# Kernel tuning notes

Hardware: AMD Instinct MI355X
Metric: run time of the kernel (lower is better)

Reference implementation:

```python
import jax, jax.numpy as jnp
import numpy as np

HEAD_DIM = 64
SCALE = HEAD_DIM ** -0.5
NUM_HEADS = 16


def setup_inputs() -> dict:
    key = jax.random.key(0)
    k1, k2, k3, k4 = jax.random.split(key, 4)
    dim = 1024
    query = jax.random.normal(k1, (8, 512, dim), dtype=jnp.float32)
    memory = jax.random.normal(k2, (8, 512, dim), dtype=jnp.float32)
    # nn.Linear weights are [out, in]; scale like default init
    W_Q = jax.random.normal(k3, (dim, dim), dtype=jnp.float32) * (dim ** -0.5)
    W_K = jax.random.normal(k4, (dim, dim), dtype=jnp.float32) * (dim ** -0.5)
    return {"query": query, "memory": memory, "W_Q": W_Q, "W_K": W_K}


def reference(query, memory, W_Q, W_K):
    # Q: [K, Lq, E], K: [B, Lk, E]  (E = H * D)
    Q = query @ W_Q.T
    Km = memory @ W_K.T
    Kb, Lq, E = Q.shape
    Bb, Lk, _ = Km.shape
    Qh = Q.reshape(Kb, Lq, NUM_HEADS, HEAD_DIM).transpose(0, 2, 1, 3)  # K H q D
    Kh = Km.reshape(Bb, Lk, NUM_HEADS, HEAD_DIM).transpose(0, 2, 1, 3)  # B H k D
    # logits: [B, K, H, q, k]
    logits = jnp.einsum('ahqd,bhkd->bahqk', Qh, Kh) * SCALE
    energies = jax.nn.logsumexp(logits, axis=-2) / SCALE  # [B, K, H, k]
    energies = energies.mean(axis=1)  # [B, H, k]
    return energies
```

## Files before the change

### kernel.cpp

```cpp
#include <hip/hip_runtime.h>
#include <hip/hip_bf16.h>

typedef short short8 __attribute__((ext_vector_type(8)));
typedef float f32x4 __attribute__((ext_vector_type(4)));
typedef unsigned short u16;

__device__ __forceinline__ unsigned short f2bf(float f) {
  unsigned int u = __float_as_uint(f);
  u += 0x7fffu + ((u >> 16) & 1u);
  return (unsigned short)(u >> 16);
}

__device__ __forceinline__ void glds16(const void* g, void* l) {
  __builtin_amdgcn_global_load_lds(
      (const __attribute__((address_space(1))) unsigned int*)g,
      (__attribute__((address_space(3))) unsigned int*)l, 16, 0, 0);
}

__global__ __launch_bounds__(256) void prep(const float4* __restrict__ q,
                                            const float4* __restrict__ m,
                                            const float4* __restrict__ wq,
                                            const float4* __restrict__ wk,
                                            ushort4* __restrict__ qb,
                                            ushort4* __restrict__ mb,
                                            ushort4* __restrict__ wqb,
                                            ushort4* __restrict__ wkb,
                                            float4* __restrict__ out0) {
  const int i = blockIdx.x * 256 + threadIdx.x;
  const float c = 0.18033688011112042f;
  if (i < 1048576) {
    float4 v = q[i];
    ushort4 o; o.x = f2bf(v.x); o.y = f2bf(v.y); o.z = f2bf(v.z); o.w = f2bf(v.w);
    qb[i] = o;
  } else if (i < 2097152) {
    float4 v = m[i - 1048576];
    ushort4 o; o.x = f2bf(v.x); o.y = f2bf(v.y); o.z = f2bf(v.z); o.w = f2bf(v.w);
    mb[i - 1048576] = o;
  } else if (i < 2359296) {
    float4 v = wq[i - 2097152];
    ushort4 o; o.x = f2bf(v.x * c); o.y = f2bf(v.y * c); o.z = f2bf(v.z * c); o.w = f2bf(v.w * c);
    wqb[i - 2097152] = o;
  } else if (i < 2621440) {
    float4 v = wk[i - 2359296];
    ushort4 o; o.x = f2bf(v.x); o.y = f2bf(v.y); o.z = f2bf(v.z); o.w = f2bf(v.w);
    wkb[i - 2359296] = o;
  } else if (i < 2637824) {
    out0[i - 2621440] = (float4){0.f, 0.f, 0.f, 0.f};
  }
}

__global__ __launch_bounds__(256) void gemm_bt2(const u16* __restrict__ A0,
                                                const u16* __restrict__ B0,
                                                u16* __restrict__ C0,
                                                const u16* __restrict__ A1,
                                                const u16* __restrict__ B1,
                                                u16* __restrict__ C1) {
  __shared__ u16 As[128 * 64];
  __shared__ u16 Bs[128 * 64];
  const u16* A = blockIdx.z ? A1 : A0;
  const u16* B = blockIdx.z ? B1 : B0;
  u16* C = blockIdx.z ? C1 : C0;
  const int t = threadIdx.x;
  const int lane = t & 63, wave = t >> 6;
  const int l15 = lane & 15, quad = lane >> 4;
  const int mb = blockIdx.y * 128, nb = blockIdx.x * 128;
  const int wm = (wave & 1) * 64, wn = (wave >> 1) * 64;

  const int srow = lane >> 3;
  const int scol = ((lane & 7) ^ srow) * 8;

  f32x4 acc[4][4];
#pragma unroll
  for (int i = 0; i < 4; i++)
#pragma unroll
    for (int j = 0; j < 4; j++) acc[i][j] = (f32x4){0.f, 0.f, 0.f, 0.f};

  for (int kb = 0; kb < 1024; kb += 64) {
#pragma unroll
    for (int j = 0; j < 4; j++) {
      const int mi_ = wave * 4 + j;
      const int row = mi_ * 8 + srow;
      glds16(A + (size_t)(mb + row) * 1024 + kb + scol, &As[mi_ * 512 + lane * 8]);
      glds16(B + (size_t)(nb + row) * 1024 + kb + scol, &Bs[mi_ * 512 + lane * 8]);
    }
    __syncthreads();
#pragma unroll
    for (int kk = 0; kk < 2; kk++) {
      const int cb = kk * 4;
      const int sw = l15 & 7;
      short8 af[4], bfr[4];
#pragma unroll
      for (int mi = 0; mi < 4; mi++)
        af[mi] = *(const short8*)&As[(wm + mi * 16 + l15) * 64 + ((cb + quad) ^ sw) * 8];
#pragma unroll
      for (int ni = 0; ni < 4; ni++)
        bfr[ni] = *(const short8*)&Bs[(wn + ni * 16 + l15) * 64 + ((cb + quad) ^ sw) * 8];
#pragma unroll
      for (int mi = 0; mi < 4; mi++)
#pragma unroll
        for (int ni = 0; ni < 4; ni++)
          acc[mi][ni] = __builtin_amdgcn_mfma_f32_16x16x32_bf16(
              af[mi], bfr[ni], acc[mi][ni], 0, 0, 0);
    }
    __syncthreads();
  }
#pragma unroll
  for (int mi = 0; mi < 4; mi++)
#pragma unroll
    for (int r = 0; r < 4; r++) {
      const int row = mb + wm + mi * 16 + quad * 4 + r;
      const size_t base = (size_t)row * 1024 + nb + wn;
#pragma unroll
      for (int ni = 0; ni < 4; ni++)
        C[base + ni * 16 + l15] = f2bf(acc[mi][ni][r]);
    }
}

__global__ __launch_bounds__(256) void attn_lse2(const u16* __restrict__ Qp,
                                                 const u16* __restrict__ Kp,
                                                 float* __restrict__ out) {
  __shared__ u16 qs[64 * 64];
  const int t = threadIdx.x;
  const int lane = t & 63, wave = t >> 6;
  const int l15 = lane & 15, quad = lane >> 4;
  const int kt = blockIdx.x & 1, aa = blockIdx.x >> 1;
  const int h = blockIdx.y, b = blockIdx.z;
  const int kwave = kt * 256 + wave * 64;

  short8 klo[4], khi[4];
#pragma unroll
  for (int tt = 0; tt < 4; tt++) {
    const short8* kg = (const short8*)(Kp + (size_t)(b * 512 + kwave + tt * 16 + l15) * 1024
                                       + h * 64 + quad * 8);
    klo[tt] = kg[0];
    khi[tt] = kg[4];
  }

  const int srow = lane >> 3;
  const int scol = ((lane & 7) ^ srow) * 8;
  const u16* qbase = Qp + (size_t)(aa * 512) * 1024 + h * 64;

  float cs0 = 0.f, cs1 = 0.f, cs2 = 0.f, cs3 = 0.f;

  for (int q0 = 0; q0 < 512; q0 += 64) {
    __syncthreads();
#pragma unroll
    for (int j = 0; j < 2; j++) {
      const int mi_ = wave * 2 + j;
      const int row = q0 + mi_ * 8 + srow;
      glds16(qbase + (size_t)row * 1024 + scol, &qs[mi_ * 512 + lane * 8]);
    }
    __syncthreads();
#pragma unroll
    for (int qt = 0; qt < 4; qt++) {
      const int rbase = (qt * 16 + l15) * 64;
      const int sw = l15 & 7;
      short8 alo = *(const short8*)&qs[rbase + (quad ^ sw) * 8];
      short8 ahi = *(const short8*)&qs[rbase + ((4 + quad) ^ sw) * 8];
      f32x4 ac0 = (f32x4){0.f, 0.f, 0.f, 0.f};
      f32x4 ac1 = ac0, ac2 = ac0, ac3 = ac0;
      ac0 = __builtin_amdgcn_mfma_f32_16x16x32_bf16(alo, klo[0], ac0, 0, 0, 0);
      ac0 = __builtin_amdgcn_mfma_f32_16x16x32_bf16(ahi, khi[0], ac0, 0, 0, 0);
      ac1 = __builtin_amdgcn_mfma_f32_16x16x32_bf16(alo, klo[1], ac1, 0, 0, 0);
      ac1 = __builtin_amdgcn_mfma_f32_16x16x32_bf16(ahi, khi[1], ac1, 0, 0, 0);
      ac2 = __builtin_amdgcn_mfma_f32_16x16x32_bf16(alo, klo[2], ac2, 0, 0, 0);
      ac2 = __builtin_amdgcn_mfma_f32_16x16x32_bf16(ahi, khi[2], ac2, 0, 0, 0);
      ac3 = __builtin_amdgcn_mfma_f32_16x16x32_bf16(alo, klo[3], ac3, 0, 0, 0);
      ac3 = __builtin_amdgcn_mfma_f32_16x16x32_bf16(ahi, khi[3], ac3, 0, 0, 0);
#pragma unroll
      for (int r = 0; r < 4; r++) {
        cs0 += exp2f(ac0[r]);
        cs1 += exp2f(ac1[r]);
        cs2 += exp2f(ac2[r]);
        cs3 += exp2f(ac3[r]);
      }
    }
  }
  cs0 += __shfl_xor(cs0, 16); cs0 += __shfl_xor(cs0, 32);
  cs1 += __shfl_xor(cs1, 16); cs1 += __shfl_xor(cs1, 32);
  cs2 += __shfl_xor(cs2, 16); cs2 += __shfl_xor(cs2, 32);
  cs3 += __shfl_xor(cs3, 16); cs3 += __shfl_xor(cs3, 32);
  const float v = quad == 0 ? cs0 : quad == 1 ? cs1 : quad == 2 ? cs2 : cs3;
  atomicAdd(out + (size_t)b * 8192 + h * 512 + kwave + quad * 16 + l15, __logf(v));
}

extern "C" void kernel_launch(void* const* d_in, const int* in_sizes, int n_in,
                              void* d_out, int out_size, void* d_ws, size_t ws_size,
                              hipStream_t stream) {
  const float* query  = (const float*)d_in[0];
  const float* memory = (const float*)d_in[1];
  const float* wq     = (const float*)d_in[2];
  const float* wk     = (const float*)d_in[3];
  float* out = (float*)d_out;

  char* ws = (char*)d_ws;
  const size_t MB = 1024 * 1024;
  u16* qb  = (u16*)(ws);
  u16* mb_ = (u16*)(ws + 8  * MB);
  u16* wqb = (u16*)(ws + 16 * MB);
  u16* wkb = (u16*)(ws + 18 * MB);
  u16* Qp  = (u16*)(ws + 20 * MB);
  u16* Kp  = (u16*)(ws + 28 * MB);

  prep<<<10304, 256, 0, stream>>>((const float4*)query, (const float4*)memory,
                                  (const float4*)wq, (const float4*)wk,
                                  (ushort4*)qb, (ushort4*)mb_, (ushort4*)wqb,
                                  (ushort4*)wkb, (float4*)d_out);
  gemm_bt2<<<dim3(8, 32, 2), 256, 0, stream>>>(qb, wqb, Qp, mb_, wkb, Kp);
  attn_lse2<<<dim3(16, 16, 8), 256, 0, stream>>>(Qp, Kp, out);
}
```

Before: 177.1 us.

## Shrink GEMM M-tile, double-buffer Q tiles in attention, use raw exp2

The projection GEMM now uses 64x128 tiles instead of 128x128, doubling the grid to 1024 blocks so more CUs are busy. The attention kernel double-buffers the Q tile in LDS, prefetching the next tile while computing the current one, which drops one barrier per iteration. It also hoists the swizzle index math and swaps exp2f for the raw hardware exp2 builtin. The trade-offs are less data reuse per GEMM block, twice the LDS in attention, and an exp2 with slightly different precision and edge-case handling.

```diff
diff --git a/kernel.cpp b/kernel.cpp
--- a/kernel.cpp
+++ b/kernel.cpp
@@ -55,7 +55,7 @@
                                                 const u16* __restrict__ A1,
                                                 const u16* __restrict__ B1,
                                                 u16* __restrict__ C1) {
-  __shared__ u16 As[128 * 64];
+  __shared__ u16 As[64 * 64];
   __shared__ u16 Bs[128 * 64];
   const u16* A = blockIdx.z ? A1 : A0;
   const u16* B = blockIdx.z ? B1 : B0;
@@ -63,40 +63,45 @@
   const int t = threadIdx.x;
   const int lane = t & 63, wave = t >> 6;
   const int l15 = lane & 15, quad = lane >> 4;
-  const int mb = blockIdx.y * 128, nb = blockIdx.x * 128;
-  const int wm = (wave & 1) * 64, wn = (wave >> 1) * 64;
+  const int mb = blockIdx.y * 64, nb = blockIdx.x * 128;
+  const int wm = (wave & 1) * 32, wn = (wave >> 1) * 64;
 
   const int srow = lane >> 3;
   const int scol = ((lane & 7) ^ srow) * 8;
 
-  f32x4 acc[4][4];
-#pragma unroll
-  for (int i = 0; i < 4; i++)
+  f32x4 acc[2][4];
+#pragma unroll
+  for (int i = 0; i < 2; i++)
 #pragma unroll
     for (int j = 0; j < 4; j++) acc[i][j] = (f32x4){0.f, 0.f, 0.f, 0.f};
 
   for (int kb = 0; kb < 1024; kb += 64) {
+#pragma unroll
+    for (int j = 0; j < 2; j++) {
+      const int mi_ = wave * 2 + j;
+      glds16(A + (size_t)(mb + mi_ * 8 + srow) * 1024 + kb + scol,
+             &As[mi_ * 512 + lane * 8]);
+    }
 #pragma unroll
     for (int j = 0; j < 4; j++) {
       const int mi_ = wave * 4 + j;
-      const int row = mi_ * 8 + srow;
-      glds16(A + (size_t)(mb + row) * 1024 + kb + scol, &As[mi_ * 512 + lane * 8]);
-      glds16(B + (size_t)(nb + row) * 1024 + kb + scol, &Bs[mi_ * 512 + lane * 8]);
+      glds16(B + (size_t)(nb + mi_ * 8 + srow) * 1024 + kb + scol,
+             &Bs[mi_ * 512 + lane * 8]);
     }
     __syncthreads();
 #pragma unroll
     for (int kk = 0; kk < 2; kk++) {
       const int cb = kk * 4;
       const int sw = l15 & 7;
-      short8 af[4], bfr[4];
-#pragma unroll
-      for (int mi = 0; mi < 4; mi++)
+      short8 af[2], bfr[4];
+#pragma unroll
+      for (int mi = 0; mi < 2; mi++)
         af[mi] = *(const short8*)&As[(wm + mi * 16 + l15) * 64 + ((cb + quad) ^ sw) * 8];
 #pragma unroll
       for (int ni = 0; ni < 4; ni++)
         bfr[ni] = *(const short8*)&Bs[(wn + ni * 16 + l15) * 64 + ((cb + quad) ^ sw) * 8];
 #pragma unroll
-      for (int mi = 0; mi < 4; mi++)
+      for (int mi = 0; mi < 2; mi++)
 #pragma unroll
         for (int ni = 0; ni < 4; ni++)
           acc[mi][ni] = __builtin_amdgcn_mfma_f32_16x16x32_bf16(
@@ -105,7 +110,7 @@
     __syncthreads();
   }
 #pragma unroll
-  for (int mi = 0; mi < 4; mi++)
+  for (int mi = 0; mi < 2; mi++)
 #pragma unroll
     for (int r = 0; r < 4; r++) {
       const int row = mb + wm + mi * 16 + quad * 4 + r;
@@ -119,7 +124,7 @@
 __global__ __launch_bounds__(256) void attn_lse2(const u16* __restrict__ Qp,
                                                  const u16* __restrict__ Kp,
                                                  float* __restrict__ out) {
-  __shared__ u16 qs[64 * 64];
+  __shared__ u16 qs[2][64 * 64];
   const int t = threadIdx.x;
   const int lane = t & 63, wave = t >> 6;
   const int l15 = lane & 15, quad = lane >> 4;
@@ -140,23 +145,34 @@
   const int scol = ((lane & 7) ^ srow) * 8;
   const u16* qbase = Qp + (size_t)(aa * 512) * 1024 + h * 64;
 
+  const int sw = l15 & 7;
+  const int colLo = (quad ^ sw) * 8;
+  const int colHi = ((4 + quad) ^ sw) * 8;
+  const int rrow = l15 * 64;
+
   float cs0 = 0.f, cs1 = 0.f, cs2 = 0.f, cs3 = 0.f;
 
-  for (int q0 = 0; q0 < 512; q0 += 64) {
+#pragma unroll
+  for (int j = 0; j < 2; j++) {
+    const int mi_ = wave * 2 + j;
+    glds16(qbase + (size_t)(mi_ * 8 + srow) * 1024 + scol, &qs[0][mi_ * 512 + lane * 8]);
+  }
+
+  for (int i = 0; i < 8; i++) {
     __syncthreads();
-#pragma unroll
-    for (int j = 0; j < 2; j++) {
-      const int mi_ = wave * 2 + j;
-      const int row = q0 + mi_ * 8 + srow;
-      glds16(qbase + (size_t)row * 1024 + scol, &qs[mi_ * 512 + lane * 8]);
-    }
-    __syncthreads();
+    if (i < 7) {
+#pragma unroll
+      for (int j = 0; j < 2; j++) {
+        const int mi_ = wave * 2 + j;
+        glds16(qbase + (size_t)((i + 1) * 64 + mi_ * 8 + srow) * 1024 + scol,
+               &qs[(i + 1) & 1][mi_ * 512 + lane * 8]);
+      }
+    }
+    const u16* buf = qs[i & 1];
 #pragma unroll
     for (int qt = 0; qt < 4; qt++) {
-      const int rbase = (qt * 16 + l15) * 64;
-      const int sw = l15 & 7;
-      short8 alo = *(const short8*)&qs[rbase + (quad ^ sw) * 8];
-      short8 ahi = *(const short8*)&qs[rbase + ((4 + quad) ^ sw) * 8];
+      short8 alo = *(const short8*)&buf[qt * 1024 + rrow + colLo];
+      short8 ahi = *(const short8*)&buf[qt * 1024 + rrow + colHi];
       f32x4 ac0 = (f32x4){0.f, 0.f, 0.f, 0.f};
       f32x4 ac1 = ac0, ac2 = ac0, ac3 = ac0;
       ac0 = __builtin_amdgcn_mfma_f32_16x16x32_bf16(alo, klo[0], ac0, 0, 0, 0);
@@ -169,10 +185,10 @@
       ac3 = __builtin_amdgcn_mfma_f32_16x16x32_bf16(ahi, khi[3], ac3, 0, 0, 0);
 #pragma unroll
       for (int r = 0; r < 4; r++) {
-        cs0 += exp2f(ac0[r]);
-        cs1 += exp2f(ac1[r]);
-        cs2 += exp2f(ac2[r]);
-        cs3 += exp2f(ac3[r]);
+        cs0 += __builtin_amdgcn_exp2f(ac0[r]);
+        cs1 += __builtin_amdgcn_exp2f(ac1[r]);
+        cs2 += __builtin_amdgcn_exp2f(ac2[r]);
+        cs3 += __builtin_amdgcn_exp2f(ac3[r]);
       }
     }
   }
@@ -206,6 +222,6 @@
                                   (const float4*)wq, (const float4*)wk,
                                   (ushort4*)qb, (ushort4*)mb_, (ushort4*)wqb,
                                   (ushort4*)wkb, (float4*)d_out);
-  gemm_bt2<<<dim3(8, 32, 2), 256, 0, stream>>>(qb, wqb, Qp, mb_, wkb, Kp);
+  gemm_bt2<<<dim3(8, 64, 2), 256, 0, stream>>>(qb, wqb, Qp, mb_, wkb, Kp);
   attn_lse2<<<dim3(16, 16, 8), 256, 0, stream>>>(Qp, Kp, out);
 }
```

Measured after the change: 156.7 us. 1.13x faster.
